# Kernel optimization log

Measured on AMD Instinct MI355X. Metric: run time of the kernel, lower is better.

Reference implementation:

```python
import jax, jax.numpy as jnp
import numpy as np

NUM_HEADS = 8
HEAD_DIM = 128
ATTN_SCALE = 0.12


def _rotary_tables(T, head_dim, dtype=jnp.float32):
    # modded-nanogpt half-truncated RoPE: rotate only first half of freq slots
    quarter = head_dim // 4
    angular = (1.0 / 1024.0) ** jnp.linspace(0.0, 1.0, quarter, dtype=dtype)
    angular = jnp.concatenate([angular, jnp.zeros(quarter, dtype=dtype)])  # [head_dim//2]
    t = jnp.arange(T, dtype=dtype)
    theta = t[:, None] * angular[None, :]  # [T, head_dim//2]
    return jnp.cos(theta), jnp.sin(theta)


def _apply_rotary(x, cos, sin):
    # x: [B, T, H, D]; cos/sin: [T, D//2]
    x1, x2 = jnp.split(x, 2, axis=-1)
    c = cos[None, :, None, :]
    s = sin[None, :, None, :]
    y1 = x1 * c + x2 * s
    y2 = -x1 * s + x2 * c
    return jnp.concatenate([y1, y2], axis=-1)


def _rms_norm(x):
    eps = jnp.asarray(jnp.finfo(x.dtype).eps, x.dtype)
    var = jnp.mean(jnp.square(x), axis=-1, keepdims=True)
    return x * jax.lax.rsqrt(var + eps)


def setup_inputs() -> dict:
    key = jax.random.key(0)
    k1, k2, k3, k4, k5 = jax.random.split(key, 5)
    B, T, D = 1, 4096, 1024
    hdim = NUM_HEADS * HEAD_DIM
    std = 0.5 * D ** (-0.5)
    x = jax.random.normal(k1, (B, T, D), dtype=jnp.float32)
    ve = jax.random.normal(k2, (B, T, hdim), dtype=jnp.float32)
    qkv_w = jax.random.normal(k3, (3, hdim, D), dtype=jnp.float32) * std
    lambdas = jnp.array([0.5, 0.5], dtype=jnp.float32)
    c_proj_w = jax.random.normal(k5, (D, hdim), dtype=jnp.float32) * std
    return {"x": x, "ve": ve, "qkv_w": qkv_w, "lambdas": lambdas, "c_proj_w": c_proj_w}


def reference(x, ve, qkv_w, lambdas, c_proj_w):
    B, T, D = x.shape
    H, Hd = NUM_HEADS, HEAD_DIM
    # QKV projection: qkv_w [3, H*Hd, D]
    qkv = jnp.einsum('btd,ckd->btck', x, qkv_w)  # [B, T, 3, H*Hd]
    qkv = qkv.reshape(B, T, 3, H, Hd)
    q, k, v = qkv[:, :, 0], qkv[:, :, 1], qkv[:, :, 2]  # [B, T, H, Hd]
    # QK RMSNorm
    q = _rms_norm(q)
    k = _rms_norm(k)
    # RoPE
    cos, sin = _rotary_tables(T, Hd, dtype=x.dtype)
    q = _apply_rotary(q, cos, sin)
    k = _apply_rotary(k, cos, sin)
    # value-embedding lambda mix
    v = lambdas[0] * v + lambdas[1] * ve.reshape(B, T, H, Hd)
    # causal attention with fixed scale 0.12 (block-causal FlexAttention mask)
    scores = jnp.einsum('bthd,bshd->bhts', q, k) * ATTN_SCALE  # [B, H, T, T]
    causal = jnp.tril(jnp.ones((T, T), dtype=bool))
    scores = jnp.where(causal[None, None], scores, jnp.asarray(-jnp.inf, scores.dtype))
    probs = jax.nn.softmax(scores, axis=-1)
    y = jnp.einsum('bhts,bshd->bthd', probs, v)  # [B, T, H, Hd]
    y = y.reshape(B, T, H * Hd)
    return y @ c_proj_w.T  # [B, T, D]
```

## Files before the change

kernel.cpp:

```cpp
#include <hip/hip_runtime.h>

typedef __bf16 bf16;
typedef __bf16 bf16x8 __attribute__((ext_vector_type(8)));
typedef __bf16 bf16x4 __attribute__((ext_vector_type(4)));
typedef float f32x4 __attribute__((ext_vector_type(4)));

#define GLL16(gp, lp)                                                          \
  __builtin_amdgcn_global_load_lds(                                            \
      (const __attribute__((address_space(1))) unsigned int*)(gp),             \
      (__attribute__((address_space(3))) unsigned int*)(lp), 16, 0, 0)

__global__ __launch_bounds__(256) void cast3_f32_bf16(
    const float* __restrict__ a, bf16* __restrict__ oa, int na4,
    const float* __restrict__ b, bf16* __restrict__ ob, int nb4,
    const float* __restrict__ c, bf16* __restrict__ oc, int nc4) {
  int i = blockIdx.x * blockDim.x + threadIdx.x;
  int stride = gridDim.x * blockDim.x;
  int total = na4 + nb4 + nc4;
  for (; i < total; i += stride) {
    const float4* src;
    bf16x4* dst;
    int j = i;
    if (j < na4) {
      src = (const float4*)a + j; dst = (bf16x4*)oa + j;
    } else if ((j -= na4) < nb4) {
      src = (const float4*)b + j; dst = (bf16x4*)ob + j;
    } else {
      j -= nb4;
      src = (const float4*)c + j; dst = (bf16x4*)oc + j;
    }
    float4 v = *src;
    bf16x4 o;
    o[0] = (bf16)v.x; o[1] = (bf16)v.y; o[2] = (bf16)v.z; o[3] = (bf16)v.w;
    *dst = o;
  }
}

template <int K, int LDC, typename CT>
__global__ __launch_bounds__(256) void gemm_bt(
    const bf16* __restrict__ A, const bf16* __restrict__ B,
    CT* __restrict__ C) {
  __shared__ __align__(16) bf16 As[128 * 64];
  __shared__ __align__(16) bf16 Bs[128 * 64];
  const int tid  = threadIdx.x;
  const int lane = tid & 63;
  const int wave = tid >> 6;
  const int ln15 = lane & 15, quad = lane >> 4;
  const int wm = wave >> 1, wn = wave & 1;
  const int m0 = blockIdx.y * 128, n0 = blockIdx.x * 128;

  f32x4 acc[4][4] = {};

  for (int k0 = 0; k0 < K; k0 += 64) {
    __syncthreads();
#pragma unroll
    for (int j = 0; j < 4; ++j) {
      int gbase = j * 256 + wave * 64;
      int g = gbase + lane;
      int r = g >> 3, c = (g & 7) ^ (r & 7);
      GLL16(A + (size_t)(m0 + r) * K + k0 + c * 8, As + (size_t)gbase * 8);
    }
#pragma unroll
    for (int j = 0; j < 4; ++j) {
      int gbase = j * 256 + wave * 64;
      int g = gbase + lane;
      int r = g >> 3, c = (g & 7) ^ (r & 7);
      GLL16(B + (size_t)(n0 + r) * K + k0 + c * 8, Bs + (size_t)gbase * 8);
    }
    __syncthreads();
#pragma unroll
    for (int kk = 0; kk < 2; ++kk) {
      bf16x8 af[4], bfr[4];
#pragma unroll
      for (int mi = 0; mi < 4; ++mi) {
        int m = wm * 64 + mi * 16 + ln15;
        int cg = kk * 4 + quad;
        af[mi] = *(const bf16x8*)(As + (m * 8 + (cg ^ (m & 7))) * 8);
      }
#pragma unroll
      for (int ni = 0; ni < 4; ++ni) {
        int n = wn * 64 + ni * 16 + ln15;
        int cg = kk * 4 + quad;
        bfr[ni] = *(const bf16x8*)(Bs + (n * 8 + (cg ^ (n & 7))) * 8);
      }
#pragma unroll
      for (int mi = 0; mi < 4; ++mi)
#pragma unroll
        for (int ni = 0; ni < 4; ++ni)
          acc[mi][ni] = __builtin_amdgcn_mfma_f32_16x16x32_bf16(
              af[mi], bfr[ni], acc[mi][ni], 0, 0, 0);
    }
  }
#pragma unroll
  for (int mi = 0; mi < 4; ++mi)
#pragma unroll
    for (int ni = 0; ni < 4; ++ni)
#pragma unroll
      for (int r = 0; r < 4; ++r) {
        int row = m0 + wm * 64 + mi * 16 + quad * 4 + r;
        int col = n0 + wn * 64 + ni * 16 + ln15;
        C[(size_t)row * LDC + col] = (CT)acc[mi][ni][r];
      }
}

__global__ __launch_bounds__(256) void qkv_post(
    const bf16* __restrict__ qkv, const float* __restrict__ ve,
    const float* __restrict__ lambdas, bf16* __restrict__ qn,
    bf16* __restrict__ kn, bf16* __restrict__ vt) {
  const int h  = blockIdx.x;
  const int t0 = blockIdx.y * 64;
  const int tid = threadIdx.x;
  const int wave = tid >> 6, lane = tid & 63;
  __shared__ __align__(16) float tile[64][129];

  const int j = lane;
  float cth = 1.0f, sth = 0.0f;
  for (int i = 0; i < 16; ++i) {
    int t = t0 + wave * 16 + i;
    if (j < 32) {
      float ang = exp2f((float)j * (-10.0f / 31.0f));
      float th = (float)t * ang;
      __sincosf(th, &sth, &cth);
    }
#pragma unroll
    for (int qk = 0; qk < 2; ++qk) {
      const bf16* row = qkv + (size_t)t * 3072 + qk * 1024 + h * 128;
      float x1 = (float)row[j], x2 = (float)row[j + 64];
      float ss = x1 * x1 + x2 * x2;
#pragma unroll
      for (int m = 1; m < 64; m <<= 1) ss += __shfl_xor(ss, m, 64);
      float rinv = rsqrtf(ss * (1.0f / 128.0f) + 1.1920929e-7f);
      if (qk == 0) rinv *= 0.12f;
      float y1 = (x1 * cth + x2 * sth) * rinv;
      float y2 = (x2 * cth - x1 * sth) * rinv;
      bf16* orow = (qk == 0 ? qn : kn) + (size_t)t * 1024 + h * 128;
      orow[j] = (bf16)y1;
      orow[j + 64] = (bf16)y2;
    }
  }

  float l0 = lambdas[0], l1 = lambdas[1];
  for (int c = 0; c < 32; ++c) {
    int idx = c * 256 + tid;
    int d = idx & 127, tl = idx >> 7;
    int t = t0 + tl;
    float v = (float)qkv[(size_t)t * 3072 + 2048 + h * 128 + d];
    float vev = ve[(size_t)t * 1024 + h * 128 + d];
    tile[tl][d] = l0 * v + l1 * vev;
  }
  __syncthreads();
  for (int c = 0; c < 32; ++c) {
    int idx = c * 256 + tid;
    int tl = idx & 63, d = idx >> 6;
    vt[((size_t)(h * 128 + d)) * 4096 + t0 + tl] = (bf16)tile[tl][d];
  }
}

__global__ __launch_bounds__(256, 2) void flash_attn(
    const bf16* __restrict__ qn, const bf16* __restrict__ kn,
    const bf16* __restrict__ vt, bf16* __restrict__ y) {
  const int halfg = blockIdx.x >> 8;
  const int idx = blockIdx.x & 255;
  const int h = idx & 7;
  const int p = idx >> 3;
  const int qtile = halfg ? p : 63 - p;
  const int tid = threadIdx.x;
  const int wave = tid >> 6, lane = tid & 63;
  const int ln15 = lane & 15, quad = lane >> 4;
  const int ln7 = ln15 & 7;

  __shared__ __align__(16) bf16 Ks[2 * 64 * 128];
  __shared__ __align__(16) bf16 Vs[2 * 128 * 64];
  __shared__ __align__(16) bf16 P[64 * 64];
  __shared__ float rsb[4][64];

  const int q0 = qtile * 64;
  const int nkv = qtile + 1;

  bf16x8 qf[4][4];
#pragma unroll
  for (int nf = 0; nf < 4; ++nf) {
    const bf16* qb = qn + (size_t)(q0 + nf * 16 + ln15) * 1024 + h * 128 + quad * 8;
#pragma unroll
    for (int ks = 0; ks < 4; ++ks) qf[nf][ks] = *(const bf16x8*)(qb + ks * 32);
  }

  f32x4 acc_o[2][4] = {};
  float rs[4] = {0.f, 0.f, 0.f, 0.f};

  auto prefetch = [&](int kt, int buf) {
    const int kv0 = kt * 64;
    bf16* ks = Ks + buf * (64 * 128);
    bf16* vs = Vs + buf * (128 * 64);
#pragma unroll
    for (int jj = 0; jj < 4; ++jj) {
      int gbase = jj * 256 + wave * 64;
      int g = gbase + lane;
      int r = g >> 4, c = (g & 15) ^ (r & 15);
      GLL16(kn + (size_t)(kv0 + r) * 1024 + h * 128 + c * 8,
            ks + (size_t)gbase * 8);
    }
#pragma unroll
    for (int jj = 0; jj < 4; ++jj) {
      int gbase = jj * 256 + wave * 64;
      int g = gbase + lane;
      int d = g >> 3, c = (g & 7) ^ (d & 7);
      GLL16(vt + ((size_t)(h * 128 + d)) * 4096 + kv0 + c * 8,
            vs + (size_t)gbase * 8);
    }
  };

  prefetch(0, 0);

  for (int kt = 0; kt < nkv; ++kt) {
    const int kv0 = kt * 64;
    __syncthreads();
    if (kt + 1 < nkv) prefetch(kt + 1, (kt + 1) & 1);
    const bf16* ksb = Ks + (kt & 1) * (64 * 128);
    const bf16* vsb = Vs + (kt & 1) * (128 * 64);

    f32x4 accs[4] = {};
#pragma unroll
    for (int ks = 0; ks < 4; ++ks) {
      bf16x8 a = *(const bf16x8*)(
          ksb + ((wave * 16 + ln15) * 16 + ((ks * 4 + quad) ^ ln15)) * 8);
#pragma unroll
      for (int nf = 0; nf < 4; ++nf)
        accs[nf] =
            __builtin_amdgcn_mfma_f32_16x16x32_bf16(a, qf[nf][ks], accs[nf], 0, 0, 0);
    }

    const bool diag = (kt == nkv - 1);
    const int kvbase = kv0 + wave * 16 + quad * 4;
#pragma unroll
    for (int nf = 0; nf < 4; ++nf) {
      const int q = q0 + nf * 16 + ln15;
      bf16x4 pk;
#pragma unroll
      for (int r = 0; r < 4; ++r) {
        float pe = __expf(accs[nf][r]);
        if (diag && kvbase + r > q) pe = 0.f;
        rs[nf] += pe;
        pk[r] = (bf16)pe;
      }
      int gp = (wave * 2 + (quad >> 1)) ^ ln7;
      *(bf16x4*)(P + ((nf * 16 + ln15) * 8 + gp) * 8 + 4 * (quad & 1)) = pk;
    }
    __syncthreads();

#pragma unroll
    for (int ks2 = 0; ks2 < 2; ++ks2) {
      bf16x8 pf[4];
#pragma unroll
      for (int nf = 0; nf < 4; ++nf)
        pf[nf] = *(const bf16x8*)(
            P + ((nf * 16 + ln15) * 8 + ((ks2 * 4 + quad) ^ ln7)) * 8);
#pragma unroll
      for (int mf = 0; mf < 2; ++mf) {
        bf16x8 a = *(const bf16x8*)(
            vsb + ((wave * 32 + mf * 16 + ln15) * 8 + ((ks2 * 4 + quad) ^ ln7)) * 8);
#pragma unroll
        for (int nf = 0; nf < 4; ++nf)
          acc_o[mf][nf] =
              __builtin_amdgcn_mfma_f32_16x16x32_bf16(a, pf[nf], acc_o[mf][nf], 0, 0, 0);
      }
    }
  }

#pragma unroll
  for (int nf = 0; nf < 4; ++nf) {
    rs[nf] += __shfl_xor(rs[nf], 16, 64);
    rs[nf] += __shfl_xor(rs[nf], 32, 64);
  }
  if (lane < 16) {
#pragma unroll
    for (int nf = 0; nf < 4; ++nf) rsb[wave][nf * 16 + ln15] = rs[nf];
  }
  __syncthreads();
  float inv[4];
#pragma unroll
  for (int nf = 0; nf < 4; ++nf)
    inv[nf] = 1.0f / (rsb[0][nf * 16 + ln15] + rsb[1][nf * 16 + ln15] +
                      rsb[2][nf * 16 + ln15] + rsb[3][nf * 16 + ln15]);

#pragma unroll
  for (int mf = 0; mf < 2; ++mf)
#pragma unroll
    for (int nf = 0; nf < 4; ++nf) {
      bf16x4 o;
#pragma unroll
      for (int r = 0; r < 4; ++r) o[r] = (bf16)(acc_o[mf][nf][r] * inv[nf]);
      *(bf16x4*)(y + (size_t)(q0 + nf * 16 + ln15) * 1024 + h * 128 +
                 wave * 32 + mf * 16 + quad * 4) = o;
    }
}

extern "C" void kernel_launch(void* const* d_in, const int* in_sizes, int n_in,
                              void* d_out, int out_size, void* d_ws,
                              size_t ws_size, hipStream_t stream) {
  const float* x       = (const float*)d_in[0];
  const float* ve      = (const float*)d_in[1];
  const float* qkv_w   = (const float*)d_in[2];
  const float* lambdas = (const float*)d_in[3];
  const float* c_proj  = (const float*)d_in[4];
  float* out = (float*)d_out;

  char* ws = (char*)d_ws;
  bf16* qkv   = (bf16*)ws;
  bf16* xbf   = (bf16*)(ws + 25165824);
  bf16* wqkv  = (bf16*)(ws + 33554432);
  bf16* wproj = (bf16*)(ws + 39845888);
  bf16* qn    = (bf16*)(ws + 41943040);
  bf16* kn    = (bf16*)(ws + 50331648);
  bf16* vt    = (bf16*)(ws + 58720256);
  bf16* yb    = (bf16*)(ws + 67108864);

  cast3_f32_bf16<<<2048, 256, 0, stream>>>(x, xbf, 4194304 / 4, qkv_w, wqkv,
                                           3145728 / 4, c_proj, wproj,
                                           1048576 / 4);

  gemm_bt<1024, 3072, bf16><<<dim3(24, 32), 256, 0, stream>>>(xbf, wqkv, qkv);

  qkv_post<<<dim3(8, 64), 256, 0, stream>>>(qkv, ve, lambdas, qn, kn, vt);

  flash_attn<<<512, 256, 0, stream>>>(qn, kn, vt, yb);

  gemm_bt<1024, 1024, float><<<dim3(8, 32), 256, 0, stream>>>(yb, wproj, out);
}
```

Baseline: 255.1 us.

## Switch flash attention to 32x32 MFMA with register-resident P and split-KV waves

Rewrites the attention inner loop to use 32x32x16 bf16 MFMAs, with each wave owning a 32-query by 32-key quadrant instead of 16x16 fragments. The probability tile is no longer staged through shared memory: it is packed into bf16 pairs and exchanged between half-waves with cross-lane shuffles, which removes the P buffer and one barrier per KV tile. The two key-half waves each hold partial output accumulators, which are combined at the end through shared memory reused from the K buffer. The cost is a larger accumulator footprint per wave and an extra reduction step in the epilogue, which raises register pressure.

Result: no change. 252.3 us (-1.1%).

```diff
diff --git a/kernel.cpp b/kernel.cpp
--- a/kernel.cpp
+++ b/kernel.cpp
@@ -3,7 +3,10 @@
 typedef __bf16 bf16;
 typedef __bf16 bf16x8 __attribute__((ext_vector_type(8)));
 typedef __bf16 bf16x4 __attribute__((ext_vector_type(4)));
+typedef __bf16 bf16x2 __attribute__((ext_vector_type(2)));
 typedef float f32x4 __attribute__((ext_vector_type(4)));
+typedef float f32x16 __attribute__((ext_vector_type(16)));
+typedef int i32x4 __attribute__((ext_vector_type(4)));
 
 #define GLL16(gp, lp)                                                          \
   __builtin_amdgcn_global_load_lds(                                            \
@@ -166,32 +169,31 @@
   const int qtile = halfg ? p : 63 - p;
   const int tid = threadIdx.x;
   const int wave = tid >> 6, lane = tid & 63;
-  const int ln15 = lane & 15, quad = lane >> 4;
-  const int ln7 = ln15 & 7;
-
-  __shared__ __align__(16) bf16 Ks[2 * 64 * 128];
-  __shared__ __align__(16) bf16 Vs[2 * 128 * 64];
-  __shared__ __align__(16) bf16 P[64 * 64];
-  __shared__ float rsb[4][64];
+  const int l31 = lane & 31, hl = lane >> 5;
+  const int qi = wave >> 1, ki = wave & 1;
+
+  __shared__ __align__(16) bf16 Ks[2][64 * 128];
+  __shared__ __align__(16) bf16 Vs[2][128 * 64];
+  __shared__ float rsb[2][2][32];
 
   const int q0 = qtile * 64;
   const int nkv = qtile + 1;
-
-  bf16x8 qf[4][4];
-#pragma unroll
-  for (int nf = 0; nf < 4; ++nf) {
-    const bf16* qb = qn + (size_t)(q0 + nf * 16 + ln15) * 1024 + h * 128 + quad * 8;
-#pragma unroll
-    for (int ks = 0; ks < 4; ++ks) qf[nf][ks] = *(const bf16x8*)(qb + ks * 32);
-  }
-
-  f32x4 acc_o[2][4] = {};
-  float rs[4] = {0.f, 0.f, 0.f, 0.f};
+  const int qg = q0 + qi * 32 + l31;
+
+  bf16x8 qf[8];
+  {
+    const bf16* qb = qn + (size_t)qg * 1024 + h * 128 + hl * 8;
+#pragma unroll
+    for (int f = 0; f < 8; ++f) qf[f] = *(const bf16x8*)(qb + f * 16);
+  }
+
+  f32x16 acc_o[4] = {};
+  float rs = 0.0f;
 
   auto prefetch = [&](int kt, int buf) {
     const int kv0 = kt * 64;
-    bf16* ks = Ks + buf * (64 * 128);
-    bf16* vs = Vs + buf * (128 * 64);
+    bf16* ks = &Ks[buf][0];
+    bf16* vs = &Vs[buf][0];
 #pragma unroll
     for (int jj = 0; jj < 4; ++jj) {
       int gbase = jj * 256 + wave * 64;
@@ -216,83 +218,99 @@
     const int kv0 = kt * 64;
     __syncthreads();
     if (kt + 1 < nkv) prefetch(kt + 1, (kt + 1) & 1);
-    const bf16* ksb = Ks + (kt & 1) * (64 * 128);
-    const bf16* vsb = Vs + (kt & 1) * (128 * 64);
-
-    f32x4 accs[4] = {};
-#pragma unroll
-    for (int ks = 0; ks < 4; ++ks) {
-      bf16x8 a = *(const bf16x8*)(
-          ksb + ((wave * 16 + ln15) * 16 + ((ks * 4 + quad) ^ ln15)) * 8);
-#pragma unroll
-      for (int nf = 0; nf < 4; ++nf)
-        accs[nf] =
-            __builtin_amdgcn_mfma_f32_16x16x32_bf16(a, qf[nf][ks], accs[nf], 0, 0, 0);
+    const bf16* ksb = &Ks[kt & 1][0];
+    const bf16* vsb = &Vs[kt & 1][0];
+
+    f32x16 accs = {};
+    const int krow = ki * 32 + l31;
+#pragma unroll
+    for (int f = 0; f < 8; ++f) {
+      bf16x8 a =
+          *(const bf16x8*)(ksb + (krow * 16 + ((2 * f + hl) ^ (krow & 15))) * 8);
+      accs = __builtin_amdgcn_mfma_f32_32x32x16_bf16(a, qf[f], accs, 0, 0, 0);
     }
 
     const bool diag = (kt == nkv - 1);
-    const int kvbase = kv0 + wave * 16 + quad * 4;
-#pragma unroll
-    for (int nf = 0; nf < 4; ++nf) {
-      const int q = q0 + nf * 16 + ln15;
-      bf16x4 pk;
-#pragma unroll
-      for (int r = 0; r < 4; ++r) {
-        float pe = __expf(accs[nf][r]);
-        if (diag && kvbase + r > q) pe = 0.f;
-        rs[nf] += pe;
-        pk[r] = (bf16)pe;
-      }
-      int gp = (wave * 2 + (quad >> 1)) ^ ln7;
-      *(bf16x4*)(P + ((nf * 16 + ln15) * 8 + gp) * 8 + 4 * (quad & 1)) = pk;
-    }
-    __syncthreads();
-
-#pragma unroll
-    for (int ks2 = 0; ks2 < 2; ++ks2) {
-      bf16x8 pf[4];
-#pragma unroll
-      for (int nf = 0; nf < 4; ++nf)
-        pf[nf] = *(const bf16x8*)(
-            P + ((nf * 16 + ln15) * 8 + ((ks2 * 4 + quad) ^ ln7)) * 8);
-#pragma unroll
-      for (int mf = 0; mf < 2; ++mf) {
+    float pe[16];
+#pragma unroll
+    for (int r = 0; r < 16; ++r) {
+      int kvl = (r & 3) + 8 * (r >> 2) + 4 * hl;
+      float v = __expf(accs[r]);
+      if (diag && (kv0 + ki * 32 + kvl) > qg) v = 0.0f;
+      rs += v;
+      pe[r] = v;
+    }
+    int pk[8];
+#pragma unroll
+    for (int g = 0; g < 8; ++g) {
+      bf16x2 t;
+      t[0] = (bf16)pe[2 * g];
+      t[1] = (bf16)pe[2 * g + 1];
+      pk[g] = __builtin_bit_cast(int, t);
+    }
+
+    bf16x8 pf[2];
+#pragma unroll
+    for (int c = 0; c < 2; ++c) {
+      int sh0 = __shfl_xor(pk[4 * c + 0], 32, 64);
+      int sh1 = __shfl_xor(pk[4 * c + 1], 32, 64);
+      int sh2 = __shfl_xor(pk[4 * c + 2], 32, 64);
+      int sh3 = __shfl_xor(pk[4 * c + 3], 32, 64);
+      int own0 = hl ? pk[4 * c + 2] : pk[4 * c + 0];
+      int own1 = hl ? pk[4 * c + 3] : pk[4 * c + 1];
+      int par0 = hl ? sh2 : sh0;
+      int par1 = hl ? sh3 : sh1;
+      i32x4 dv;
+      dv[0] = hl ? par0 : own0;
+      dv[1] = hl ? par1 : own1;
+      dv[2] = hl ? own0 : par0;
+      dv[3] = hl ? own1 : par1;
+      pf[c] = __builtin_bit_cast(bf16x8, dv);
+    }
+
+#pragma unroll
+    for (int dt = 0; dt < 4; ++dt) {
+      int vrow = dt * 32 + l31;
+#pragma unroll
+      for (int c = 0; c < 2; ++c) {
         bf16x8 a = *(const bf16x8*)(
-            vsb + ((wave * 32 + mf * 16 + ln15) * 8 + ((ks2 * 4 + quad) ^ ln7)) * 8);
-#pragma unroll
-        for (int nf = 0; nf < 4; ++nf)
-          acc_o[mf][nf] =
-              __builtin_amdgcn_mfma_f32_16x16x32_bf16(a, pf[nf], acc_o[mf][nf], 0, 0, 0);
-      }
-    }
-  }
-
-#pragma unroll
-  for (int nf = 0; nf < 4; ++nf) {
-    rs[nf] += __shfl_xor(rs[nf], 16, 64);
-    rs[nf] += __shfl_xor(rs[nf], 32, 64);
-  }
-  if (lane < 16) {
-#pragma unroll
-    for (int nf = 0; nf < 4; ++nf) rsb[wave][nf * 16 + ln15] = rs[nf];
-  }
+            vsb + (vrow * 8 + ((4 * ki + 2 * c + hl) ^ (vrow & 7))) * 8);
+        acc_o[dt] =
+            __builtin_amdgcn_mfma_f32_32x32x16_bf16(a, pf[c], acc_o[dt], 0, 0, 0);
+      }
+    }
+  }
+
+  rs += __shfl_xor(rs, 32, 64);
   __syncthreads();
-  float inv[4];
-#pragma unroll
-  for (int nf = 0; nf < 4; ++nf)
-    inv[nf] = 1.0f / (rsb[0][nf * 16 + ln15] + rsb[1][nf * 16 + ln15] +
-                      rsb[2][nf * 16 + ln15] + rsb[3][nf * 16 + ln15]);
-
-#pragma unroll
-  for (int mf = 0; mf < 2; ++mf)
-#pragma unroll
-    for (int nf = 0; nf < 4; ++nf) {
-      bf16x4 o;
-#pragma unroll
-      for (int r = 0; r < 4; ++r) o[r] = (bf16)(acc_o[mf][nf][r] * inv[nf]);
-      *(bf16x4*)(y + (size_t)(q0 + nf * 16 + ln15) * 1024 + h * 128 +
-                 wave * 32 + mf * 16 + quad * 4) = o;
-    }
+  if (lane < 32) rsb[qi][ki][l31] = rs;
+  float* ob = (float*)&Ks[0][0];
+  if (ki == 1) {
+#pragma unroll
+    for (int dt = 0; dt < 4; ++dt)
+#pragma unroll
+      for (int r = 0; r < 16; ++r) {
+        int d = dt * 32 + (r & 3) + 8 * (r >> 2) + 4 * hl;
+        ob[qi * 4096 + l31 * 128 + d] = acc_o[dt][r];
+      }
+  }
+  __syncthreads();
+  if (ki == 0) {
+    float inv = 1.0f / (rsb[qi][0][l31] + rsb[qi][1][l31]);
+#pragma unroll
+    for (int dt = 0; dt < 4; ++dt)
+#pragma unroll
+      for (int rg = 0; rg < 4; ++rg) {
+        bf16x4 o;
+#pragma unroll
+        for (int j = 0; j < 4; ++j) {
+          int r = rg * 4 + j;
+          int d = dt * 32 + 4 * hl + 8 * rg + j;
+          o[j] = (bf16)((acc_o[dt][r] + ob[qi * 4096 + l31 * 128 + d]) * inv);
+        }
+        *(bf16x4*)(y + (size_t)qg * 1024 + h * 128 + dt * 32 + 4 * hl + 8 * rg) = o;
+      }
+  }
 }
 
 extern "C" void kernel_launch(void* const* d_in, const int* in_sizes, int n_in,
```
